# Kernel tuning notes

Hardware: AMD Instinct MI355X
Metric: run time of the kernel (lower is better)

## Reference

```python
import jax, jax.numpy as jnp
import numpy as np

N_CELLS = 19683   # 27**3 lattice
K = 26            # Moore-neighborhood max_neighbors
D = 128           # state_size
HG = 64           # gating hidden
CNF_STEPS = 3     # integration_steps
DT = 0.1


def setup_inputs() -> dict:
    key = jax.random.key(0)
    ks = jax.random.split(key, 12)
    s = lambda fan_in: 1.0 / np.sqrt(fan_in)
    return {
        "current_state": jax.random.normal(ks[0], (N_CELLS, D), jnp.float32),
        "neighbor_states": jax.random.normal(ks[1], (N_CELLS, K, D), jnp.float32),
        "conn_type": jax.random.randint(ks[2], (N_CELLS, K), 0, 3, jnp.int32),
        "W_local": jax.random.normal(ks[3], (2 * D, D), jnp.float32) * s(2 * D),
        "b_local": jnp.zeros((D,), jnp.float32),
        "W_msg": jax.random.normal(ks[4], (2 * D, D), jnp.float32) * s(2 * D),
        "b_msg": jnp.zeros((D,), jnp.float32),
        "W_upd": jax.random.normal(ks[5], (2 * D, D), jnp.float32) * s(2 * D),
        "b_upd": jnp.zeros((D,), jnp.float32),
        "W_cnf": jax.random.normal(ks[6], (2 * D, D), jnp.float32) * s(2 * D),
        "b_cnf": jnp.zeros((D,), jnp.float32),
        "W_g1": jax.random.normal(ks[7], (D, HG), jnp.float32) * s(D),
        "b_g1": jnp.zeros((HG,), jnp.float32),
        "W_g2": jax.random.normal(ks[8], (HG, 3), jnp.float32) * s(HG),
        "b_g2": jnp.zeros((3,), jnp.float32),
    }


def _masked_mean(nbr, mask):
    # nbr: [N,K,D], mask: [N,K] float -> [N,D]
    cnt = jnp.maximum(mask.sum(-1, keepdims=True), 1.0)
    return jnp.einsum("nkd,nk->nd", nbr, mask) / cnt


def reference(current_state, neighbor_states, conn_type,
              W_local, b_local, W_msg, b_msg, W_upd, b_upd,
              W_cnf, b_cnf, W_g1, b_g1, W_g2, b_g2):
    cur = current_state                       # [N,D]
    nbr = neighbor_states                     # [N,K,D]
    m_l = (conn_type == 0).astype(cur.dtype)  # local mask   [N,K]
    m_f = (conn_type == 1).astype(cur.dtype)  # functional
    m_d = (conn_type == 2).astype(cur.dtype)  # distant

    # --- local expert: SimpleLinear over [cell, mean(local neighbors)] ---
    agg_l = _masked_mean(nbr, m_l)
    local_out = jnp.tanh(jnp.concatenate([cur, agg_l], -1) @ W_local + b_local)

    # --- functional expert: GNN message passing ---
    cur_b = jnp.broadcast_to(cur[:, None, :], nbr.shape)          # [N,K,D]
    edge_in = jnp.concatenate([cur_b, nbr], -1)                   # [N,K,2D]
    msgs = jax.nn.relu(edge_in @ W_msg + b_msg)                   # [N,K,D]
    agg_msg = _masked_mean(msgs, m_f)                             # [N,D]
    func_out = jnp.tanh(jnp.concatenate([cur, agg_msg], -1) @ W_upd + b_upd)

    # --- distant expert: lightweight CNF (fixed-step Euler) ---
    agg_d = _masked_mean(nbr, m_d)

    def euler_step(s, _):
        ds = jnp.tanh(jnp.concatenate([s, agg_d], -1) @ W_cnf + b_cnf)
        return s + DT * ds, None

    distant_out, _ = jax.lax.scan(euler_step, cur, None, length=CNF_STEPS)

    # --- gating network: softmax over 3 experts ---
    gates = jax.nn.softmax(jax.nn.relu(cur @ W_g1 + b_g1) @ W_g2 + b_g2, -1)  # [N,3]

    out = (gates[:, 0:1] * local_out
           + gates[:, 1:2] * func_out
           + gates[:, 2:3] * distant_out)
    return out
```

## Files before the change

### kernel.cpp

```cpp
#include <hip/hip_runtime.h>
#include <math.h>

#define NC 19683
#define KN 26
#define DD 128
#define HGN 64
#define LDSB 136
#define DTC 0.1f
#define CPW 8
#define CPB 32

using bf8v = __attribute__((ext_vector_type(8))) short;
using f4v  = __attribute__((ext_vector_type(4))) float;

static __device__ __forceinline__ unsigned short f2bf(float x) {
    union { float f; unsigned u; } v; v.f = x;
    unsigned r = v.u + 0x7fffu + ((v.u >> 16) & 1u);
    return (unsigned short)(r >> 16);
}
static __device__ __forceinline__ unsigned pk2(float a, float b) {
    return ((unsigned)f2bf(a)) | (((unsigned)f2bf(b)) << 16);
}

__global__ __launch_bounds__(256) void k_prep(const float* __restrict__ Wl,
    const float* __restrict__ Wm, const float* __restrict__ Wu,
    const float* __restrict__ Wc, const float* __restrict__ Wg1,
    unsigned short* __restrict__ WT, unsigned short* __restrict__ WgT)
{
    int idx = blockIdx.x * 256 + threadIdx.x;
    if (idx < 131072) {
        int m = idx >> 15;
        int r = idx & 32767;
        int j = r >> 8;
        int i = r & 255;
        const float* src = (m == 0) ? Wl : (m == 1) ? Wm : (m == 2) ? Wu : Wc;
        WT[idx] = f2bf(src[i * DD + j]);
    } else {
        int idx2 = idx - 131072;
        int col = idx2 >> 7;
        int k = idx2 & 127;
        WgT[idx2] = f2bf(Wg1[k * HGN + col]);
    }
}

__global__ __launch_bounds__(256, 2) void kE(const float* __restrict__ cur,
    const float* __restrict__ nbr, const int* __restrict__ conn,
    const unsigned short* __restrict__ WT, const float* __restrict__ b_msg,
    unsigned short* __restrict__ agg_l, unsigned short* __restrict__ agg_m,
    unsigned short* __restrict__ agg_d)
{
    __shared__ __align__(16) unsigned short Wt[128 * LDSB];
    __shared__ __align__(16) unsigned short Anb[110 * LDSB];
    __shared__ float Pbuf[CPB * DD];
    int t = threadIdx.x;
    int n0 = blockIdx.x * CPB;
    int w = t >> 6, lane = t & 63;
    int lm = lane & 15, lq = lane >> 4;
    int j2 = lane * 2;

    for (int p = 0; p < 8; ++p) {
        int idx = p * 256 + t;
        int r = idx >> 6, c2 = (idx & 63) * 2;
        float2 v = {0.f, 0.f};
        if (n0 + r < NC) v = *(const float2*)&cur[(size_t)(n0 + r) * DD + c2];
        *(unsigned*)&Anb[r * LDSB + c2] = pk2(v.x, v.y);
    }
    {
        const unsigned short* Wm1 = WT + 32768;
        for (int p = 0; p < 8; ++p) {
            int ch = p * 256 + t;
            int j = ch >> 4, i8 = (ch & 15) * 8;
            *(bf8v*)&Wt[j * LDSB + i8] = *(const bf8v*)&Wm1[j * 256 + i8];
        }
    }
    __syncthreads();

    int cw0 = n0 + w * CPW;
    float2 vv[KN];
    int ct = 3;
    {
        bool a = cw0 < NC;
        if (a && lane < KN) ct = conn[(size_t)cw0 * KN + lane];
        const float* bp = nbr + (size_t)(a ? cw0 : 0) * KN * DD + j2;
        #pragma unroll
        for (int k = 0; k < KN; ++k) {
            float2 v = {0.f, 0.f};
            if (a) v = *(const float2*)&bp[(size_t)k * DD];
            vv[k] = v;
        }
    }

    for (int nt = 0; nt < 2; ++nt) {
        int col0 = w * 32 + nt * 16;
        float bm = b_msg[col0 + lm];
        for (int mt2 = 0; mt2 < 2; ++mt2) {
            f4v acc = {0.f, 0.f, 0.f, 0.f};
            #pragma unroll
            for (int s = 0; s < 4; ++s) {
                bf8v a = *(const bf8v*)&Anb[(mt2 * 16 + lm) * LDSB + s * 32 + lq * 8];
                bf8v b = *(const bf8v*)&Wt[(col0 + lm) * LDSB + s * 32 + lq * 8];
                acc = __builtin_amdgcn_mfma_f32_16x16x32_bf16(a, b, acc, 0, 0, 0);
            }
            for (int r = 0; r < 4; ++r) {
                int row = mt2 * 16 + lq * 4 + r;
                Pbuf[row * DD + col0 + lm] = acc[r] + bm;
            }
        }
    }
    __syncthreads();

    {
        const unsigned short* Wm2 = WT + 32768 + 128;
        for (int p = 0; p < 8; ++p) {
            int ch = p * 256 + t;
            int j = ch >> 4, i8 = (ch & 15) * 8;
            *(bf8v*)&Wt[j * LDSB + i8] = *(const bf8v*)&Wm2[j * 256 + i8];
        }
    }
    __syncthreads();

    int abase = w * KN;
    for (int i = 0; i < CPW; ++i) {
        int n = cw0 + i;
        if (n >= NC) break;
        unsigned long long mlb = __ballot(ct == 0);
        unsigned long long mfb = __ballot(ct == 1);
        unsigned long long mdb = __ballot(ct == 2);
        float icl = 1.f / fmaxf((float)__builtin_popcountll(mlb), 1.f);
        float icf = 1.f / fmaxf((float)__builtin_popcountll(mfb), 1.f);
        float icd = 1.f / fmaxf((float)__builtin_popcountll(mdb), 1.f);
        float slx = 0.f, sly = 0.f, sdx = 0.f, sdy = 0.f;
        #pragma unroll
        for (int k = 0; k < KN; ++k) {
            float2 v = vv[k];
            if ((mlb >> k) & 1) { slx += v.x; sly += v.y; }
            if ((mdb >> k) & 1) { sdx += v.x; sdy += v.y; }
            *(unsigned*)&Anb[(abase + k) * LDSB + j2] = pk2(v.x, v.y);
        }
        *(unsigned*)&agg_l[(size_t)n * DD + j2] = pk2(slx * icl, sly * icl);
        *(unsigned*)&agg_d[(size_t)n * DD + j2] = pk2(sdx * icd, sdy * icd);

        if (i + 1 < CPW) {
            int n2 = cw0 + i + 1;
            bool a2 = n2 < NC;
            int ct2 = 3;
            if (a2 && lane < KN) ct2 = conn[(size_t)n2 * KN + lane];
            const float* bp2 = nbr + (size_t)(a2 ? n2 : 0) * KN * DD + j2;
            #pragma unroll
            for (int k = 0; k < KN; ++k) {
                float2 v = {0.f, 0.f};
                if (a2) v = *(const float2*)&bp2[(size_t)k * DD];
                vv[k] = v;
            }
            ct = ct2;
        }

        bf8v afr[2][4];
        #pragma unroll
        for (int mt2 = 0; mt2 < 2; ++mt2)
            #pragma unroll
            for (int s = 0; s < 4; ++s)
                afr[mt2][s] = *(const bf8v*)&Anb[(abase + mt2 * 16 + lm) * LDSB + s * 32 + lq * 8];

        int prow = (w * CPW + i) * DD;
        __builtin_amdgcn_s_setprio(1);
        #pragma unroll
        for (int nt = 0; nt < 8; ++nt) {
            float pv = Pbuf[prow + nt * 16 + lm];
            f4v a0 = {0.f, 0.f, 0.f, 0.f}, a1 = {0.f, 0.f, 0.f, 0.f};
            #pragma unroll
            for (int s = 0; s < 4; ++s) {
                bf8v b = *(const bf8v*)&Wt[(nt * 16 + lm) * LDSB + s * 32 + lq * 8];
                a0 = __builtin_amdgcn_mfma_f32_16x16x32_bf16(afr[0][s], b, a0, 0, 0, 0);
                a1 = __builtin_amdgcn_mfma_f32_16x16x32_bf16(afr[1][s], b, a1, 0, 0, 0);
            }
            float msum = 0.f;
            #pragma unroll
            for (int r = 0; r < 4; ++r) {
                int rr = lq * 4 + r;
                if ((mfb >> rr) & 1) msum += fmaxf(pv + a0[r], 0.f);
                int rr2 = 16 + lq * 4 + r;
                if ((mfb >> rr2) & 1) msum += fmaxf(pv + a1[r], 0.f);
            }
            msum += __shfl_xor(msum, 16, 64);
            msum += __shfl_xor(msum, 32, 64);
            if (lane < 16) agg_m[(size_t)n * DD + nt * 16 + lane] = f2bf(msum * icf);
        }
        __builtin_amdgcn_s_setprio(0);
    }
}

__global__ __launch_bounds__(256) void kC(const float* __restrict__ cur,
    const unsigned short* __restrict__ WT, const unsigned short* __restrict__ WgT,
    const unsigned short* __restrict__ agg_l, const unsigned short* __restrict__ agg_m,
    const unsigned short* __restrict__ agg_d,
    const float* __restrict__ b_local, const float* __restrict__ b_upd,
    const float* __restrict__ b_cnf, const float* __restrict__ bg1,
    const float* __restrict__ Wg2, const float* __restrict__ bg2,
    float* __restrict__ out)
{
    __shared__ __align__(16) unsigned short Wl[128][LDSB];
    __shared__ __align__(16) unsigned short Xc[32][LDSB];
    __shared__ __align__(16) unsigned short Xa[32][LDSB];
    __shared__ float hrelu[32][HGN + 4];
    __shared__ float glds[32][4];
    __shared__ float bl[DD], bu[DD], bc[DD];
    __shared__ float Wg2s[HGN * 3];
    __shared__ float bg2s[4];
    int t = threadIdx.x;
    int n0 = blockIdx.x * 32;
    int w = t >> 6, lane = t & 63;
    int mt = w & 1, colh = w >> 1;
    int lm = lane & 15, lq = lane >> 4;

    auto stageW = [&](int m, int koff) {
        const unsigned short* src = WT + m * 32768 + koff;
        for (int p = 0; p < 8; ++p) {
            int ch = p * 256 + t;
            int j = ch >> 4, i8 = (ch & 15) * 8;
            *(bf8v*)&Wl[j][i8] = *(const bf8v*)&src[j * 256 + i8];
        }
    };
    auto stageXa = [&](const unsigned short* src) {
        for (int p = 0; p < 2; ++p) {
            int idx = p * 256 + t;
            int r = idx >> 4, c8 = (idx & 15) * 8;
            bf8v v = {0, 0, 0, 0, 0, 0, 0, 0};
            if (n0 + r < NC) v = *(const bf8v*)&src[(size_t)(n0 + r) * DD + c8];
            *(bf8v*)&Xa[r][c8] = v;
        }
    };
    auto mfmaPass = [&](unsigned short (&X)[32][LDSB], f4v* acc) {
        for (int nt = 0; nt < 4; ++nt) {
            int col0 = colh * 64 + nt * 16;
            for (int s = 0; s < 4; ++s) {
                bf8v a = *(const bf8v*)&X[mt * 16 + lm][s * 32 + lq * 8];
                bf8v b = *(const bf8v*)&Wl[col0 + lm][s * 32 + lq * 8];
                acc[nt] = __builtin_amdgcn_mfma_f32_16x16x32_bf16(a, b, acc[nt], 0, 0, 0);
            }
        }
    };

    for (int p = 0; p < 8; ++p) {
        int idx = p * 256 + t;
        int r = idx >> 6, c2 = (idx & 63) * 2;
        float2 v = {0.f, 0.f};
        if (n0 + r < NC) v = *(const float2*)&cur[(size_t)(n0 + r) * DD + c2];
        *(unsigned*)&Xc[r][c2] = pk2(v.x, v.y);
    }
    for (int p = 0; p < 4; ++p) {
        int ch = p * 256 + t;
        int j = ch >> 4, i8 = (ch & 15) * 8;
        *(bf8v*)&Wl[j][i8] = *(const bf8v*)&WgT[j * 128 + i8];
    }
    if (t < 128) { bl[t] = b_local[t]; bu[t] = b_upd[t]; bc[t] = b_cnf[t]; }
    for (int i = t; i < HGN * 3; i += 256) Wg2s[i] = Wg2[i];
    if (t < 3) bg2s[t] = bg2[t];
    __syncthreads();

    {
        int col0 = w * 16;
        float bg = bg1[col0 + lm];
        for (int mt2 = 0; mt2 < 2; ++mt2) {
            f4v acc = {0.f, 0.f, 0.f, 0.f};
            for (int s = 0; s < 4; ++s) {
                bf8v a = *(const bf8v*)&Xc[mt2 * 16 + lm][s * 32 + lq * 8];
                bf8v b = *(const bf8v*)&Wl[col0 + lm][s * 32 + lq * 8];
                acc = __builtin_amdgcn_mfma_f32_16x16x32_bf16(a, b, acc, 0, 0, 0);
            }
            for (int r = 0; r < 4; ++r)
                hrelu[mt2 * 16 + lq * 4 + r][col0 + lm] = fmaxf(acc[r] + bg, 0.f);
        }
    }
    __syncthreads();

    stageW(0, 0);
    if (t < 96) {
        int r = t / 3, e = t - r * 3;
        float s = bg2s[e];
        for (int g = 0; g < HGN; ++g) s += hrelu[r][g] * Wg2s[g * 3 + e];
        glds[r][e] = s;
    }
    __syncthreads();

    if (t < 32) {
        float l0 = glds[t][0], l1 = glds[t][1], l2 = glds[t][2];
        float m = fmaxf(l0, fmaxf(l1, l2));
        float e0 = expf(l0 - m), e1 = expf(l1 - m), e2 = expf(l2 - m);
        float inv = 1.f / (e0 + e1 + e2);
        glds[t][0] = e0 * inv; glds[t][1] = e1 * inv; glds[t][2] = e2 * inv;
    }
    f4v oacc[4], acc[4];
    for (int nt = 0; nt < 4; ++nt) oacc[nt] = (f4v){0.f, 0.f, 0.f, 0.f};

    for (int nt = 0; nt < 4; ++nt) acc[nt] = (f4v){0.f, 0.f, 0.f, 0.f};
    mfmaPass(Xc, acc);
    __syncthreads();
    stageW(0, 128); stageXa(agg_l);
    __syncthreads();
    mfmaPass(Xa, acc);
    for (int nt = 0; nt < 4; ++nt) {
        int col = colh * 64 + nt * 16 + lm;
        for (int r = 0; r < 4; ++r) {
            int row = mt * 16 + lq * 4 + r;
            oacc[nt][r] += glds[row][0] * tanhf(acc[nt][r] + bl[col]);
        }
    }

    __syncthreads();
    stageW(2, 0);
    __syncthreads();
    for (int nt = 0; nt < 4; ++nt) acc[nt] = (f4v){0.f, 0.f, 0.f, 0.f};
    mfmaPass(Xc, acc);
    __syncthreads();
    stageW(2, 128); stageXa(agg_m);
    __syncthreads();
    mfmaPass(Xa, acc);
    for (int nt = 0; nt < 4; ++nt) {
        int col = colh * 64 + nt * 16 + lm;
        for (int r = 0; r < 4; ++r) {
            int row = mt * 16 + lq * 4 + r;
            oacc[nt][r] += glds[row][1] * tanhf(acc[nt][r] + bu[col]);
        }
    }

    __syncthreads();
    stageW(3, 128); stageXa(agg_d);
    __syncthreads();
    for (int nt = 0; nt < 4; ++nt) acc[nt] = (f4v){0.f, 0.f, 0.f, 0.f};
    mfmaPass(Xa, acc);
    f4v hd[4], s[4];
    for (int nt = 0; nt < 4; ++nt) {
        int col = colh * 64 + nt * 16 + lm;
        for (int r = 0; r < 4; ++r) {
            int row = mt * 16 + lq * 4 + r;
            int n = n0 + row;
            hd[nt][r] = acc[nt][r] + bc[col];
            s[nt][r] = (n < NC) ? cur[(size_t)n * DD + col] : 0.f;
        }
    }
    __syncthreads();
    stageW(3, 0);
    for (int step = 0; step < 3; ++step) {
        for (int nt = 0; nt < 4; ++nt) {
            int col = colh * 64 + nt * 16 + lm;
            for (int r = 0; r < 4; ++r) {
                int row = mt * 16 + lq * 4 + r;
                Xa[row][col] = f2bf(s[nt][r]);
            }
        }
        __syncthreads();
        for (int nt = 0; nt < 4; ++nt) acc[nt] = (f4v){0.f, 0.f, 0.f, 0.f};
        mfmaPass(Xa, acc);
        for (int nt = 0; nt < 4; ++nt)
            for (int r = 0; r < 4; ++r)
                s[nt][r] += DTC * tanhf(acc[nt][r] + hd[nt][r]);
        __syncthreads();
    }

    for (int nt = 0; nt < 4; ++nt) {
        int col = colh * 64 + nt * 16 + lm;
        for (int r = 0; r < 4; ++r) {
            int row = mt * 16 + lq * 4 + r;
            int n = n0 + row;
            if (n < NC) out[(size_t)n * DD + col] = oacc[nt][r] + glds[row][2] * s[nt][r];
        }
    }
}

extern "C" void kernel_launch(void* const* d_in, const int* in_sizes, int n_in,
                              void* d_out, int out_size, void* d_ws, size_t ws_size,
                              hipStream_t stream) {
    const float* cur     = (const float*)d_in[0];
    const float* nbr     = (const float*)d_in[1];
    const int*   conn    = (const int*)d_in[2];
    const float* W_local = (const float*)d_in[3];
    const float* b_local = (const float*)d_in[4];
    const float* W_msg   = (const float*)d_in[5];
    const float* b_msg   = (const float*)d_in[6];
    const float* W_upd   = (const float*)d_in[7];
    const float* b_upd   = (const float*)d_in[8];
    const float* W_cnf   = (const float*)d_in[9];
    const float* b_cnf   = (const float*)d_in[10];
    const float* Wg1     = (const float*)d_in[11];
    const float* bg1     = (const float*)d_in[12];
    const float* Wg2     = (const float*)d_in[13];
    const float* bg2     = (const float*)d_in[14];
    float* out = (float*)d_out;

    char* ws = (char*)d_ws;
    unsigned short* WT   = (unsigned short*)ws;
    unsigned short* WgT  = (unsigned short*)(ws + 262144);
    unsigned short* aggl = (unsigned short*)(ws + 278528);
    unsigned short* aggm = aggl + (size_t)NC * DD;
    unsigned short* aggd = aggm + (size_t)NC * DD;

    hipLaunchKernelGGL(k_prep, dim3(544), dim3(256), 0, stream,
                       W_local, W_msg, W_upd, W_cnf, Wg1, WT, WgT);
    hipLaunchKernelGGL(kE, dim3((NC + CPB - 1) / CPB), dim3(256), 0, stream,
                       cur, nbr, conn, WT, b_msg, aggl, aggm, aggd);
    hipLaunchKernelGGL(kC, dim3(616), dim3(256), 0, stream, cur, WT, WgT, aggl, aggm, aggd,
                       b_local, b_upd, b_cnf, bg1, Wg2, bg2, out);
}
```

Before: 472.2 us.

## Double-buffer neighbor prefetch two cells ahead and read W_msg1 from global

The edge kernel now keeps two register buffers of neighbor rows and prefetches the cell two steps ahead rather than one, so global loads have more time to land before they are consumed. The precompute of cur@W_msg now reads its weight half straight from global memory, which drops one LDS weight staging pass and one barrier, and loads the second weight half into LDS at the start. The s_setprio hints are removed and a sched_barrier is added. Holding a second 26-entry float2 buffer raises register pressure, which may cut occupancy below the two-blocks-per-SM launch bound or cause spills.

```diff
diff --git a/kernel.cpp b/kernel.cpp
--- a/kernel.cpp
+++ b/kernel.cpp
@@ -57,6 +57,7 @@
     int w = t >> 6, lane = t & 63;
     int lm = lane & 15, lq = lane >> 4;
     int j2 = lane * 2;
+    int cw0 = n0 + w * CPW;
 
     for (int p = 0; p < 8; ++p) {
         int idx = p * 256 + t;
@@ -66,50 +67,6 @@
         *(unsigned*)&Anb[r * LDSB + c2] = pk2(v.x, v.y);
     }
     {
-        const unsigned short* Wm1 = WT + 32768;
-        for (int p = 0; p < 8; ++p) {
-            int ch = p * 256 + t;
-            int j = ch >> 4, i8 = (ch & 15) * 8;
-            *(bf8v*)&Wt[j * LDSB + i8] = *(const bf8v*)&Wm1[j * 256 + i8];
-        }
-    }
-    __syncthreads();
-
-    int cw0 = n0 + w * CPW;
-    float2 vv[KN];
-    int ct = 3;
-    {
-        bool a = cw0 < NC;
-        if (a && lane < KN) ct = conn[(size_t)cw0 * KN + lane];
-        const float* bp = nbr + (size_t)(a ? cw0 : 0) * KN * DD + j2;
-        #pragma unroll
-        for (int k = 0; k < KN; ++k) {
-            float2 v = {0.f, 0.f};
-            if (a) v = *(const float2*)&bp[(size_t)k * DD];
-            vv[k] = v;
-        }
-    }
-
-    for (int nt = 0; nt < 2; ++nt) {
-        int col0 = w * 32 + nt * 16;
-        float bm = b_msg[col0 + lm];
-        for (int mt2 = 0; mt2 < 2; ++mt2) {
-            f4v acc = {0.f, 0.f, 0.f, 0.f};
-            #pragma unroll
-            for (int s = 0; s < 4; ++s) {
-                bf8v a = *(const bf8v*)&Anb[(mt2 * 16 + lm) * LDSB + s * 32 + lq * 8];
-                bf8v b = *(const bf8v*)&Wt[(col0 + lm) * LDSB + s * 32 + lq * 8];
-                acc = __builtin_amdgcn_mfma_f32_16x16x32_bf16(a, b, acc, 0, 0, 0);
-            }
-            for (int r = 0; r < 4; ++r) {
-                int row = mt2 * 16 + lq * 4 + r;
-                Pbuf[row * DD + col0 + lm] = acc[r] + bm;
-            }
-        }
-    }
-    __syncthreads();
-
-    {
         const unsigned short* Wm2 = WT + 32768 + 128;
         for (int p = 0; p < 8; ++p) {
             int ch = p * 256 + t;
@@ -117,15 +74,65 @@
             *(bf8v*)&Wt[j * LDSB + i8] = *(const bf8v*)&Wm2[j * 256 + i8];
         }
     }
+
+    float2 vvA[KN], vvB[KN];
+    int ctA = 3, ctB = 3;
+    {
+        int n1 = cw0;
+        bool a = n1 < NC;
+        if (a && lane < KN) ctA = conn[(size_t)n1 * KN + lane];
+        const float* bp = nbr + (size_t)(a ? n1 : 0) * KN * DD + j2;
+        #pragma unroll
+        for (int k = 0; k < KN; ++k) {
+            float2 v = {0.f, 0.f};
+            if (a) v = *(const float2*)&bp[(size_t)k * DD];
+            vvA[k] = v;
+        }
+    }
+    {
+        int n1 = cw0 + 1;
+        bool a = n1 < NC;
+        if (a && lane < KN) ctB = conn[(size_t)n1 * KN + lane];
+        const float* bp = nbr + (size_t)(a ? n1 : 0) * KN * DD + j2;
+        #pragma unroll
+        for (int k = 0; k < KN; ++k) {
+            float2 v = {0.f, 0.f};
+            if (a) v = *(const float2*)&bp[(size_t)k * DD];
+            vvB[k] = v;
+        }
+    }
+    __syncthreads();
+
+    {
+        const unsigned short* Wm1 = WT + 32768;
+        for (int nt = 0; nt < 2; ++nt) {
+            int col0 = w * 32 + nt * 16;
+            float bm = b_msg[col0 + lm];
+            const unsigned short* bb = &Wm1[(col0 + lm) * 256 + lq * 8];
+            for (int mt2 = 0; mt2 < 2; ++mt2) {
+                f4v acc = {0.f, 0.f, 0.f, 0.f};
+                #pragma unroll
+                for (int s = 0; s < 4; ++s) {
+                    bf8v a = *(const bf8v*)&Anb[(mt2 * 16 + lm) * LDSB + s * 32 + lq * 8];
+                    bf8v b = *(const bf8v*)&bb[s * 32];
+                    acc = __builtin_amdgcn_mfma_f32_16x16x32_bf16(a, b, acc, 0, 0, 0);
+                }
+                for (int r = 0; r < 4; ++r) {
+                    int row = mt2 * 16 + lq * 4 + r;
+                    Pbuf[row * DD + col0 + lm] = acc[r] + bm;
+                }
+            }
+        }
+    }
     __syncthreads();
 
     int abase = w * KN;
-    for (int i = 0; i < CPW; ++i) {
+    auto edge_cell = [&](float2 (&vv)[KN], int &ctR, int i) {
         int n = cw0 + i;
-        if (n >= NC) break;
-        unsigned long long mlb = __ballot(ct == 0);
-        unsigned long long mfb = __ballot(ct == 1);
-        unsigned long long mdb = __ballot(ct == 2);
+        if (n >= NC) return;
+        unsigned long long mlb = __ballot(ctR == 0);
+        unsigned long long mfb = __ballot(ctR == 1);
+        unsigned long long mdb = __ballot(ctR == 2);
         float icl = 1.f / fmaxf((float)__builtin_popcountll(mlb), 1.f);
         float icf = 1.f / fmaxf((float)__builtin_popcountll(mfb), 1.f);
         float icd = 1.f / fmaxf((float)__builtin_popcountll(mdb), 1.f);
@@ -140,11 +147,11 @@
         *(unsigned*)&agg_l[(size_t)n * DD + j2] = pk2(slx * icl, sly * icl);
         *(unsigned*)&agg_d[(size_t)n * DD + j2] = pk2(sdx * icd, sdy * icd);
 
-        if (i + 1 < CPW) {
-            int n2 = cw0 + i + 1;
-            bool a2 = n2 < NC;
-            int ct2 = 3;
-            if (a2 && lane < KN) ct2 = conn[(size_t)n2 * KN + lane];
+        {
+            int n2 = cw0 + i + 2;
+            bool a2 = (i + 2 < CPW) && (n2 < NC);
+            int ctn = 3;
+            if (a2 && lane < KN) ctn = conn[(size_t)n2 * KN + lane];
             const float* bp2 = nbr + (size_t)(a2 ? n2 : 0) * KN * DD + j2;
             #pragma unroll
             for (int k = 0; k < KN; ++k) {
@@ -152,8 +159,9 @@
                 if (a2) v = *(const float2*)&bp2[(size_t)k * DD];
                 vv[k] = v;
             }
-            ct = ct2;
-        }
+            ctR = ctn;
+        }
+        __builtin_amdgcn_sched_barrier(0);
 
         bf8v afr[2][4];
         #pragma unroll
@@ -163,7 +171,6 @@
                 afr[mt2][s] = *(const bf8v*)&Anb[(abase + mt2 * 16 + lm) * LDSB + s * 32 + lq * 8];
 
         int prow = (w * CPW + i) * DD;
-        __builtin_amdgcn_s_setprio(1);
         #pragma unroll
         for (int nt = 0; nt < 8; ++nt) {
             float pv = Pbuf[prow + nt * 16 + lm];
@@ -186,7 +193,11 @@
             msum += __shfl_xor(msum, 32, 64);
             if (lane < 16) agg_m[(size_t)n * DD + nt * 16 + lane] = f2bf(msum * icf);
         }
-        __builtin_amdgcn_s_setprio(0);
+    };
+
+    for (int ii = 0; ii < CPW; ii += 2) {
+        edge_cell(vvA, ctA, ii);
+        edge_cell(vvB, ctB, ii + 1);
     }
 }
 
```

Result: no change. 467.3 us (-1.0%).

## Stage neighbor tiles into LDS via async double-buffered global_load_lds

Applied to the files above, without the earlier changes.

Neighbor rows for each cell are now copied straight from global memory into swizzled, double-buffered LDS slots with async global_load_lds, and waited on with explicit vmcnt waits. This replaces the 26-entry register prefetch and the manual bf16 packing into LDS. The cell-side projection reads its A operand from global and converts it in registers, so the first weight-load phase and one barrier go away. Conversion to bf16 uses v_cvt_pk_bf16_f32. The larger single LDS arena lowers occupancy from 2 to 1 block per CU, and the hand-counted waitcnts make the code fragile.

```diff
diff --git a/kernel.cpp b/kernel.cpp
--- a/kernel.cpp
+++ b/kernel.cpp
@@ -9,9 +9,15 @@
 #define DTC 0.1f
 #define CPW 8
 #define CPB 32
+#define SLOTB 13312
 
 using bf8v = __attribute__((ext_vector_type(8))) short;
 using f4v  = __attribute__((ext_vector_type(4))) float;
+
+typedef __attribute__((address_space(1))) const void g_void;
+typedef __attribute__((address_space(3))) void l_void;
+
+#define WAITV(N) asm volatile("s_waitcnt vmcnt(" #N ")" ::: "memory")
 
 static __device__ __forceinline__ unsigned short f2bf(float x) {
     union { float f; unsigned u; } v; v.f = x;
@@ -20,6 +26,14 @@
 }
 static __device__ __forceinline__ unsigned pk2(float a, float b) {
     return ((unsigned)f2bf(a)) | (((unsigned)f2bf(b)) << 16);
+}
+static __device__ __forceinline__ bf8v cvt8(float4 lo, float4 hi) {
+    union { bf8v v; unsigned d[4]; } u;
+    asm volatile("v_cvt_pk_bf16_f32 %0, %1, %2" : "=v"(u.d[0]) : "v"(lo.x), "v"(lo.y));
+    asm volatile("v_cvt_pk_bf16_f32 %0, %1, %2" : "=v"(u.d[1]) : "v"(lo.z), "v"(lo.w));
+    asm volatile("v_cvt_pk_bf16_f32 %0, %1, %2" : "=v"(u.d[2]) : "v"(hi.x), "v"(hi.y));
+    asm volatile("v_cvt_pk_bf16_f32 %0, %1, %2" : "=v"(u.d[3]) : "v"(hi.z), "v"(hi.w));
+    return u.v;
 }
 
 __global__ __launch_bounds__(256) void k_prep(const float* __restrict__ Wl,
@@ -43,71 +57,28 @@
     }
 }
 
-__global__ __launch_bounds__(256, 2) void kE(const float* __restrict__ cur,
+__global__ __launch_bounds__(256, 1) void kE(const float* __restrict__ cur,
     const float* __restrict__ nbr, const int* __restrict__ conn,
     const unsigned short* __restrict__ WT, const float* __restrict__ b_msg,
     unsigned short* __restrict__ agg_l, unsigned short* __restrict__ agg_m,
     unsigned short* __restrict__ agg_d)
 {
-    __shared__ __align__(16) unsigned short Wt[128 * LDSB];
-    __shared__ __align__(16) unsigned short Anb[110 * LDSB];
-    __shared__ float Pbuf[CPB * DD];
+    __shared__ __align__(16) char LDSA[157696];
+    float* Pb = (float*)(LDSA + 106496);
+    unsigned short* Wt = (unsigned short*)(LDSA + 122880);
+
     int t = threadIdx.x;
     int n0 = blockIdx.x * CPB;
     int w = t >> 6, lane = t & 63;
     int lm = lane & 15, lq = lane >> 4;
-    int j2 = lane * 2;
-
-    for (int p = 0; p < 8; ++p) {
-        int idx = p * 256 + t;
-        int r = idx >> 6, c2 = (idx & 63) * 2;
-        float2 v = {0.f, 0.f};
-        if (n0 + r < NC) v = *(const float2*)&cur[(size_t)(n0 + r) * DD + c2];
-        *(unsigned*)&Anb[r * LDSB + c2] = pk2(v.x, v.y);
-    }
-    {
-        const unsigned short* Wm1 = WT + 32768;
-        for (int p = 0; p < 8; ++p) {
-            int ch = p * 256 + t;
-            int j = ch >> 4, i8 = (ch & 15) * 8;
-            *(bf8v*)&Wt[j * LDSB + i8] = *(const bf8v*)&Wm1[j * 256 + i8];
-        }
-    }
-    __syncthreads();
-
     int cw0 = n0 + w * CPW;
-    float2 vv[KN];
-    int ct = 3;
-    {
-        bool a = cw0 < NC;
-        if (a && lane < KN) ct = conn[(size_t)cw0 * KN + lane];
-        const float* bp = nbr + (size_t)(a ? cw0 : 0) * KN * DD + j2;
-        #pragma unroll
-        for (int k = 0; k < KN; ++k) {
-            float2 v = {0.f, 0.f};
-            if (a) v = *(const float2*)&bp[(size_t)k * DD];
-            vv[k] = v;
-        }
-    }
-
-    for (int nt = 0; nt < 2; ++nt) {
-        int col0 = w * 32 + nt * 16;
-        float bm = b_msg[col0 + lm];
-        for (int mt2 = 0; mt2 < 2; ++mt2) {
-            f4v acc = {0.f, 0.f, 0.f, 0.f};
-            #pragma unroll
-            for (int s = 0; s < 4; ++s) {
-                bf8v a = *(const bf8v*)&Anb[(mt2 * 16 + lm) * LDSB + s * 32 + lq * 8];
-                bf8v b = *(const bf8v*)&Wt[(col0 + lm) * LDSB + s * 32 + lq * 8];
-                acc = __builtin_amdgcn_mfma_f32_16x16x32_bf16(a, b, acc, 0, 0, 0);
-            }
-            for (int r = 0; r < 4; ++r) {
-                int row = mt2 * 16 + lq * 4 + r;
-                Pbuf[row * DD + col0 + lm] = acc[r] + bm;
-            }
-        }
-    }
-    __syncthreads();
+
+    int ctv[CPW];
+    #pragma unroll
+    for (int i = 0; i < CPW; ++i) {
+        int n = cw0 + i;
+        ctv[i] = (n < NC && lane < KN) ? conn[(size_t)n * KN + lane] : 3;
+    }
 
     {
         const unsigned short* Wm2 = WT + 32768 + 128;
@@ -117,56 +88,104 @@
             *(bf8v*)&Wt[j * LDSB + i8] = *(const bf8v*)&Wm2[j * 256 + i8];
         }
     }
-    __syncthreads();
-
-    int abase = w * KN;
+
+    {
+        const unsigned short* Wm1 = WT + 32768;
+        bf8v afrP[2][4];
+        #pragma unroll
+        for (int mt2 = 0; mt2 < 2; ++mt2) {
+            int gr = n0 + mt2 * 16 + lm;
+            if (gr >= NC) gr = NC - 1;
+            const float* rb = &cur[(size_t)gr * DD];
+            #pragma unroll
+            for (int s = 0; s < 4; ++s) {
+                float4 lo = *(const float4*)&rb[s * 32 + lq * 8];
+                float4 hi = *(const float4*)&rb[s * 32 + lq * 8 + 4];
+                afrP[mt2][s] = cvt8(lo, hi);
+            }
+        }
+        for (int nt = 0; nt < 2; ++nt) {
+            int col0 = w * 32 + nt * 16;
+            float bm = b_msg[col0 + lm];
+            const unsigned short* bb = &Wm1[(col0 + lm) * 256 + lq * 8];
+            for (int mt2 = 0; mt2 < 2; ++mt2) {
+                f4v acc = {0.f, 0.f, 0.f, 0.f};
+                #pragma unroll
+                for (int s = 0; s < 4; ++s) {
+                    bf8v b = *(const bf8v*)&bb[s * 32];
+                    acc = __builtin_amdgcn_mfma_f32_16x16x32_bf16(afrP[mt2][s], b, acc, 0, 0, 0);
+                }
+                for (int r = 0; r < 4; ++r) {
+                    int row = mt2 * 16 + lq * 4 + r;
+                    Pb[row * DD + col0 + lm] = acc[r] + bm;
+                }
+            }
+        }
+    }
+    __syncthreads();
+
+    int rlo = lane >> 5;
+    unsigned wb = (unsigned)(lane & 31) * 16;
+    auto stage = [&](int i) {
+        int nn = cw0 + i; if (nn >= NC) nn = NC - 1;
+        const char* cellbase = (const char*)(nbr + (size_t)nn * KN * DD);
+        char* slot = LDSA + (size_t)(w * 2 + (i & 1)) * SLOTB;
+        #pragma unroll
+        for (int j = 0; j < 13; ++j) {
+            int row = 2 * j + rlo;
+            const char* src = cellbase + (size_t)row * 512 + (wb ^ ((unsigned)(row & 7) << 4));
+            __builtin_amdgcn_global_load_lds((g_void*)src, (l_void*)(slot + j * 1024), 16, 0, 0);
+        }
+    };
+
+    stage(0);
     for (int i = 0; i < CPW; ++i) {
         int n = cw0 + i;
         if (n >= NC) break;
+        if (i + 1 < CPW) stage(i + 1);
+        if (i == 0) WAITV(13);
+        else if (i + 1 < CPW) WAITV(23);
+        else WAITV(10);
+        __builtin_amdgcn_sched_barrier(0);
+
+        const char* slot = LDSA + (size_t)(w * 2 + (i & 1)) * SLOTB;
+        int ct = ctv[i];
         unsigned long long mlb = __ballot(ct == 0);
         unsigned long long mfb = __ballot(ct == 1);
         unsigned long long mdb = __ballot(ct == 2);
         float icl = 1.f / fmaxf((float)__builtin_popcountll(mlb), 1.f);
         float icf = 1.f / fmaxf((float)__builtin_popcountll(mfb), 1.f);
         float icd = 1.f / fmaxf((float)__builtin_popcountll(mdb), 1.f);
+
         float slx = 0.f, sly = 0.f, sdx = 0.f, sdy = 0.f;
         #pragma unroll
         for (int k = 0; k < KN; ++k) {
-            float2 v = vv[k];
+            float2 v = *(const float2*)(slot + (size_t)k * 512 + (((unsigned)lane * 8) ^ ((unsigned)(k & 7) << 4)));
             if ((mlb >> k) & 1) { slx += v.x; sly += v.y; }
             if ((mdb >> k) & 1) { sdx += v.x; sdy += v.y; }
-            *(unsigned*)&Anb[(abase + k) * LDSB + j2] = pk2(v.x, v.y);
-        }
-        *(unsigned*)&agg_l[(size_t)n * DD + j2] = pk2(slx * icl, sly * icl);
-        *(unsigned*)&agg_d[(size_t)n * DD + j2] = pk2(sdx * icd, sdy * icd);
-
-        if (i + 1 < CPW) {
-            int n2 = cw0 + i + 1;
-            bool a2 = n2 < NC;
-            int ct2 = 3;
-            if (a2 && lane < KN) ct2 = conn[(size_t)n2 * KN + lane];
-            const float* bp2 = nbr + (size_t)(a2 ? n2 : 0) * KN * DD + j2;
-            #pragma unroll
-            for (int k = 0; k < KN; ++k) {
-                float2 v = {0.f, 0.f};
-                if (a2) v = *(const float2*)&bp2[(size_t)k * DD];
-                vv[k] = v;
-            }
-            ct = ct2;
-        }
+        }
+        *(unsigned*)&agg_l[(size_t)n * DD + lane * 2] = pk2(slx * icl, sly * icl);
+        *(unsigned*)&agg_d[(size_t)n * DD + lane * 2] = pk2(sdx * icd, sdy * icd);
 
         bf8v afr[2][4];
         #pragma unroll
-        for (int mt2 = 0; mt2 < 2; ++mt2)
+        for (int mt2 = 0; mt2 < 2; ++mt2) {
+            int row = mt2 * 16 + lm;
+            unsigned X = (unsigned)(row & 7) << 4;
+            const char* rb = slot + (size_t)row * 512;
             #pragma unroll
-            for (int s = 0; s < 4; ++s)
-                afr[mt2][s] = *(const bf8v*)&Anb[(abase + mt2 * 16 + lm) * LDSB + s * 32 + lq * 8];
+            for (int s = 0; s < 4; ++s) {
+                unsigned b0 = (unsigned)(s * 128 + lq * 32);
+                float4 lo = *(const float4*)(rb + (b0 ^ X));
+                float4 hi = *(const float4*)(rb + ((b0 + 16) ^ X));
+                afr[mt2][s] = cvt8(lo, hi);
+            }
+        }
 
         int prow = (w * CPW + i) * DD;
-        __builtin_amdgcn_s_setprio(1);
         #pragma unroll
         for (int nt = 0; nt < 8; ++nt) {
-            float pv = Pbuf[prow + nt * 16 + lm];
+            float pv = Pb[prow + nt * 16 + lm];
             f4v a0 = {0.f, 0.f, 0.f, 0.f}, a1 = {0.f, 0.f, 0.f, 0.f};
             #pragma unroll
             for (int s = 0; s < 4; ++s) {
@@ -186,7 +205,6 @@
             msum += __shfl_xor(msum, 32, 64);
             if (lane < 16) agg_m[(size_t)n * DD + nt * 16 + lane] = f2bf(msum * icf);
         }
-        __builtin_amdgcn_s_setprio(0);
     }
 }
 
```

Measured after the change: 492.2 us. 1.04x slower.
